# Performance work log

Measured on AMD Instinct MI355X. Metric: run time of the kernel, lower is better.

## Reference

```python
import jax, jax.numpy as jnp
import numpy as np

D_MODEL = 128
N_LAYERS = 2
D_STATE = 16
D_CONV = 4
EXPAND = 2
GRID = 16
D_INNER = D_MODEL * EXPAND
DT_RANK = (D_MODEL + 15) // 16  # mamba_ssm default: ceil(d_model/16) = 8
BATCH = 128
SEQ = 200


def setup_inputs() -> dict:
    key = jax.random.key(0)
    ks = jax.random.split(key, 24)
    L = N_LAYERS

    def rn(k, shape, scale=0.02):
        return jax.random.normal(k, shape, dtype=jnp.float32) * scale

    A_init = jnp.log(jnp.broadcast_to(
        jnp.arange(1, D_STATE + 1, dtype=jnp.float32), (L, D_INNER, D_STATE)))
    kan_scale = 1.0 / (np.sqrt(D_MODEL) * np.sqrt(GRID))
    return {
        "x": jax.random.normal(ks[0], (BATCH, SEQ, D_MODEL), dtype=jnp.float32),
        "in_w": rn(ks[1], (L, 2 * D_INNER, D_MODEL)),
        "out_w": rn(ks[2], (L, D_MODEL, D_INNER)),
        "conv_w_f": rn(ks[3], (L, D_INNER, D_CONV), 0.1),
        "conv_b_f": rn(ks[4], (L, D_INNER), 0.01),
        "conv_w_b": rn(ks[5], (L, D_INNER, D_CONV), 0.1),
        "conv_b_b": rn(ks[6], (L, D_INNER), 0.01),
        "xproj_w_f": rn(ks[7], (L, DT_RANK + 2 * D_STATE, D_INNER)),
        "xproj_w_b": rn(ks[8], (L, DT_RANK + 2 * D_STATE, D_INNER)),
        "dtproj_w_f": rn(ks[9], (L, D_INNER, DT_RANK), 0.1),
        "dtproj_b_f": rn(ks[10], (L, D_INNER), 0.01),
        "dtproj_w_b": rn(ks[11], (L, D_INNER, DT_RANK), 0.1),
        "dtproj_b_b": rn(ks[12], (L, D_INNER), 0.01),
        "A_log_f": A_init,
        "A_log_b": A_init,
        "D_f": jnp.ones((L, D_INNER), jnp.float32),
        "D_b": jnp.ones((L, D_INNER), jnp.float32),
        "ln1_w": jnp.ones((L, D_MODEL), jnp.float32),
        "ln1_b": jnp.zeros((L, D_MODEL), jnp.float32),
        "ln_w": jnp.ones((L, D_MODEL), jnp.float32),
        "ln_b": jnp.zeros((L, D_MODEL), jnp.float32),
        "kan_coef": jax.random.normal(ks[13], (L, 2, D_MODEL, D_MODEL, GRID), dtype=jnp.float32) * kan_scale,
    }


def _ln(x, w, b, eps=1e-12):
    u = x.mean(-1, keepdims=True)
    s = ((x - u) ** 2).mean(-1, keepdims=True)
    return w * (x - u) / jnp.sqrt(s + eps) + b


def _silu(x):
    return x * jax.nn.sigmoid(x)


def _mamba(x, in_w, out_w, conv_w, conv_b, xp_w, dt_w, dt_b, A_log, Dp):
    # x: (B, L, d_model). Faithful to mamba_ssm Mamba (bias=False proj, conv_bias=True).
    B, L, _ = x.shape
    xz = jnp.einsum('bld,ed->ble', x, in_w)          # (B, L, 2*d_inner)
    xi, z = jnp.split(xz, 2, axis=-1)
    # causal depthwise conv over L
    xp = jnp.pad(xi, ((0, 0), (D_CONV - 1, 0), (0, 0)))
    xc = sum(xp[:, k:k + L, :] * conv_w[:, k] for k in range(D_CONV)) + conv_b
    xc = _silu(xc)                                    # (B, L, d_inner)
    dbl = jnp.einsum('ble,fe->blf', xc, xp_w)         # (B, L, dt_rank+2*d_state)
    dt = jax.nn.softplus(
        jnp.einsum('blr,dr->bld', dbl[..., :DT_RANK], dt_w) + dt_b)
    Bm = dbl[..., DT_RANK:DT_RANK + D_STATE]          # (B, L, d_state)
    Cm = dbl[..., DT_RANK + D_STATE:]
    A = -jnp.exp(A_log)                               # (d_inner, d_state)

    def step(h, inp):
        dt_t, u_t, b_t, c_t = inp                     # (B,di),(B,di),(B,ds),(B,ds)
        h = jnp.exp(dt_t[:, :, None] * A) * h + (dt_t * u_t)[:, :, None] * b_t[:, None, :]
        return h, jnp.einsum('bds,bs->bd', h, c_t)

    h0 = jnp.zeros((B, D_INNER, D_STATE), x.dtype)
    _, ys = jax.lax.scan(step, h0, (jnp.moveaxis(dt, 1, 0), jnp.moveaxis(xc, 1, 0),
                                    jnp.moveaxis(Bm, 1, 0), jnp.moveaxis(Cm, 1, 0)))
    y = jnp.moveaxis(ys, 0, 1) + xc * Dp              # (B, L, d_inner)
    y = y * _silu(z)
    return jnp.einsum('ble,de->bld', y, out_w)


def _kan(x, coef):
    # coef: (2, outdim, inputdim, grid)
    shp = x.shape
    xf = x.reshape(-1, shp[-1])                       # (N, d)
    kk = jnp.arange(1, GRID + 1, dtype=x.dtype)
    ang = xf[:, :, None] * kk                         # (N, d, grid)
    y = (jnp.einsum('nig,jig->nj', jnp.cos(ang), coef[0])
         + jnp.einsum('nig,jig->nj', jnp.sin(ang), coef[1]))
    return y.reshape(shp[:-1] + (coef.shape[1],))


def reference(x, in_w, out_w, conv_w_f, conv_b_f, conv_w_b, conv_b_b,
              xproj_w_f, xproj_w_b, dtproj_w_f, dtproj_b_f, dtproj_w_b, dtproj_b_b,
              A_log_f, A_log_b, D_f, D_b, ln1_w, ln1_b, ln_w, ln_b, kan_coef):
    feats = []
    h = x
    for l in range(N_LAYERS):
        o = _ln(h, ln1_w[l], ln1_b[l])
        f = _mamba(o, in_w[l], out_w[l], conv_w_f[l], conv_b_f[l],
                   xproj_w_f[l], dtproj_w_f[l], dtproj_b_f[l], A_log_f[l], D_f[l])
        b = _mamba(o[:, ::-1], in_w[l], out_w[l], conv_w_b[l], conv_b_b[l],
                   xproj_w_b[l], dtproj_w_b[l], dtproj_b_b[l], A_log_b[l], D_b[l])[:, ::-1]
        o = _ln(f + b, ln_w[l], ln_b[l])
        o = _kan(o, kan_coef[l])  # dropout p=0.0 (eval) -> identity
        h = o + h
        feats.append(h)
    return sum(feats) / len(feats)
```

## Files before the change

### kernel.cpp

```cpp
#include <hip/hip_runtime.h>
#include <hip/hip_bf16.h>
#include <cmath>

#define BATCH 128
#define SEQ 200
#define DMODEL 128
#define DINNER 256
#define DSTATE 16
#define NTOK (BATCH * SEQ)

typedef __bf16 bf16x8 __attribute__((ext_vector_type(8)));
typedef float f32x4 __attribute__((ext_vector_type(4)));

__device__ __forceinline__ unsigned short f2bf(float f) {
  union { float f; unsigned u; } x{f};
  const unsigned r = x.u + 0x7fffu + ((x.u >> 16) & 1u);
  return (unsigned short)(r >> 16);
}
__device__ __forceinline__ float bf2f(unsigned short h) {
  union { unsigned u; float f; } x{(unsigned)h << 16};
  return x.f;
}
__device__ __forceinline__ void split2(float a, float b, unsigned& hp, unsigned& lp) {
  const unsigned short ha = f2bf(a), hb = f2bf(b);
  const float ra = a - bf2f(ha), rb = b - bf2f(hb);
  hp = (unsigned)ha | ((unsigned)hb << 16);
  lp = (unsigned)f2bf(ra) | ((unsigned)f2bf(rb) << 16);
}

template <int CTRL>
__device__ __forceinline__ float dpp_add(float v) {
  const int r = __builtin_amdgcn_update_dpp(0, __float_as_int(v), CTRL, 0xF, 0xF, true);
  return v + __int_as_float(r);
}

__device__ __forceinline__ float silu_f(float x) {
  return x / (1.f + __expf(-x));
}

__global__ __launch_bounds__(256) void ln_kernel(const float* __restrict__ in,
                                                 const float* __restrict__ w,
                                                 const float* __restrict__ b,
                                                 float* __restrict__ out) {
  const int wv = threadIdx.x >> 6;
  const int lane = threadIdx.x & 63;
  const int row = blockIdx.x * 4 + wv;
  const float2 v = *(const float2*)(in + (size_t)row * DMODEL + lane * 2);
  float s = v.x + v.y;
#pragma unroll
  for (int o = 32; o; o >>= 1) s += __shfl_xor(s, o, 64);
  const float u = s * (1.f / 128.f);
  const float dx = v.x - u, dy = v.y - u;
  float sq = dx * dx + dy * dy;
#pragma unroll
  for (int o = 32; o; o >>= 1) sq += __shfl_xor(sq, o, 64);
  const float inv = rsqrtf(sq * (1.f / 128.f) + 1e-12f);
  const float2 wv2 = *(const float2*)(w + lane * 2);
  const float2 bv2 = *(const float2*)(b + lane * 2);
  float2 o2v;
  o2v.x = fmaf(wv2.x, dx * inv, bv2.x);
  o2v.y = fmaf(wv2.y, dy * inv, bv2.y);
  *(float2*)(out + (size_t)row * DMODEL + lane * 2) = o2v;
}

__global__ __launch_bounds__(256) void wprep(const float* __restrict__ in_w,
                                             const float* __restrict__ xpwf,
                                             const float* __restrict__ xpwb,
                                             const float* __restrict__ out_w,
                                             unsigned short* __restrict__ iwH,
                                             unsigned short* __restrict__ iwL,
                                             unsigned short* __restrict__ xfH,
                                             unsigned short* __restrict__ xfL,
                                             unsigned short* __restrict__ xbH,
                                             unsigned short* __restrict__ xbL,
                                             unsigned short* __restrict__ owH,
                                             unsigned short* __restrict__ owL) {
  const int idx = blockIdx.x * 256 + threadIdx.x;
  float w;
  unsigned short *H, *L;
  int off;
  if (idx < 65536)      { w = in_w[idx];        H = iwH; L = iwL; off = idx; }
  else if (idx < 75776) { w = xpwf[idx - 65536]; H = xfH; L = xfL; off = idx - 65536; }
  else if (idx < 86016) { w = xpwb[idx - 75776]; H = xbH; L = xbL; off = idx - 75776; }
  else                  { w = out_w[idx - 86016]; H = owH; L = owL; off = idx - 86016; }
  const unsigned short h = f2bf(w);
  H[off] = h;
  L[off] = f2bf(w - bf2f(h));
}

template <int MODE>
__global__ __launch_bounds__(256) void gemm_c(const float* __restrict__ A1,
                                              const float* __restrict__ A2,
                                              const float* __restrict__ Zp,
                                              const unsigned short* __restrict__ Whi,
                                              const unsigned short* __restrict__ Wlo,
                                              float* __restrict__ C,
                                              const unsigned short* __restrict__ Whi2,
                                              const unsigned short* __restrict__ Wlo2,
                                              float* __restrict__ C2,
                                              int M, int N, int K) {
  __shared__ unsigned short AshH[64 * 40], AshL[64 * 40];
  __shared__ unsigned short BshH[128 * 40], BshL[128 * 40];
  const float* Ause = A1;
  const unsigned short* WH = Whi;
  const unsigned short* WL = Wlo;
  float* Cuse = C;
  if (MODE == 2 && blockIdx.z == 1) { Ause = A2; WH = Whi2; WL = Wlo2; Cuse = C2; }
  const int tid = threadIdx.x;
  const int m0 = blockIdx.y * 64;
  const int n0 = blockIdx.x * 128;
  const int lane = tid & 63;
  const int wid = tid >> 6;
  const int arow = lane & 15;
  const int kch = (lane >> 4) * 8;
  const int bcol = wid * 32 + (lane & 15);
  f32x4 acc[4][2] = {};
  for (int k0 = 0; k0 < K; k0 += 32) {
    __syncthreads();
    {
      const int row = tid >> 2;
      const int koff = (tid & 3) * 8;
      const int m = m0 + row;
      float4 v0 = *(const float4*)(Ause + (size_t)m * K + k0 + koff);
      float4 v1 = *(const float4*)(Ause + (size_t)m * K + k0 + koff + 4);
      if (MODE == 1) {
        const float4 u0 = *(const float4*)(A2 + (size_t)m * K + k0 + koff);
        const float4 u1 = *(const float4*)(A2 + (size_t)m * K + k0 + koff + 4);
        const float4 z0 = *(const float4*)(Zp + (size_t)m * 512 + k0 + koff);
        const float4 z1 = *(const float4*)(Zp + (size_t)m * 512 + k0 + koff + 4);
        v0.x = (v0.x + u0.x) * silu_f(z0.x);
        v0.y = (v0.y + u0.y) * silu_f(z0.y);
        v0.z = (v0.z + u0.z) * silu_f(z0.z);
        v0.w = (v0.w + u0.w) * silu_f(z0.w);
        v1.x = (v1.x + u1.x) * silu_f(z1.x);
        v1.y = (v1.y + u1.y) * silu_f(z1.y);
        v1.z = (v1.z + u1.z) * silu_f(z1.z);
        v1.w = (v1.w + u1.w) * silu_f(z1.w);
      }
      unsigned h0, l0, h1, l1, h2, l2, h3, l3;
      split2(v0.x, v0.y, h0, l0);
      split2(v0.z, v0.w, h1, l1);
      split2(v1.x, v1.y, h2, l2);
      split2(v1.z, v1.w, h3, l3);
      *(uint4*)&AshH[row * 40 + koff] = make_uint4(h0, h1, h2, h3);
      *(uint4*)&AshL[row * 40 + koff] = make_uint4(l0, l1, l2, l3);
    }
    {
      const int row = tid >> 1;
      const int koff = (tid & 1) * 16;
      const int n = n0 + row;
      uint4 wh0 = make_uint4(0, 0, 0, 0), wh1 = wh0, wl0 = wh0, wl1 = wh0;
      if (n < N) {
        wh0 = *(const uint4*)(WH + (size_t)n * K + k0 + koff);
        wh1 = *(const uint4*)(WH + (size_t)n * K + k0 + koff + 8);
        wl0 = *(const uint4*)(WL + (size_t)n * K + k0 + koff);
        wl1 = *(const uint4*)(WL + (size_t)n * K + k0 + koff + 8);
      }
      *(uint4*)&BshH[row * 40 + koff] = wh0;
      *(uint4*)&BshH[row * 40 + koff + 8] = wh1;
      *(uint4*)&BshL[row * 40 + koff] = wl0;
      *(uint4*)&BshL[row * 40 + koff + 8] = wl1;
    }
    __syncthreads();
    const bf16x8 bh0 = *(const bf16x8*)&BshH[bcol * 40 + kch];
    const bf16x8 bh1 = *(const bf16x8*)&BshH[(bcol + 16) * 40 + kch];
    const bf16x8 bl0 = *(const bf16x8*)&BshL[bcol * 40 + kch];
    const bf16x8 bl1 = *(const bf16x8*)&BshL[(bcol + 16) * 40 + kch];
#pragma unroll
    for (int g = 0; g < 4; ++g) {
      const bf16x8 ah = *(const bf16x8*)&AshH[(g * 16 + arow) * 40 + kch];
      const bf16x8 al = *(const bf16x8*)&AshL[(g * 16 + arow) * 40 + kch];
      acc[g][0] = __builtin_amdgcn_mfma_f32_16x16x32_bf16(ah, bh0, acc[g][0], 0, 0, 0);
      acc[g][0] = __builtin_amdgcn_mfma_f32_16x16x32_bf16(al, bh0, acc[g][0], 0, 0, 0);
      acc[g][0] = __builtin_amdgcn_mfma_f32_16x16x32_bf16(ah, bl0, acc[g][0], 0, 0, 0);
      acc[g][1] = __builtin_amdgcn_mfma_f32_16x16x32_bf16(ah, bh1, acc[g][1], 0, 0, 0);
      acc[g][1] = __builtin_amdgcn_mfma_f32_16x16x32_bf16(al, bh1, acc[g][1], 0, 0, 0);
      acc[g][1] = __builtin_amdgcn_mfma_f32_16x16x32_bf16(ah, bl1, acc[g][1], 0, 0, 0);
    }
  }
  const int q0 = (lane >> 4) * 4;
#pragma unroll
  for (int g = 0; g < 4; ++g)
#pragma unroll
    for (int fc = 0; fc < 2; ++fc)
#pragma unroll
      for (int q = 0; q < 4; ++q) {
        const int m = m0 + g * 16 + q0 + q;
        const int n = n0 + wid * 32 + fc * 16 + (lane & 15);
        if (n < N) Cuse[(size_t)m * N + n] = acc[g][fc][q];
      }
}

__global__ __launch_bounds__(256) void conv_silu_kernel(const float* __restrict__ xz,
                                                        const float* __restrict__ cwf,
                                                        const float* __restrict__ cbf,
                                                        const float* __restrict__ cwb,
                                                        const float* __restrict__ cbb,
                                                        float* __restrict__ xcf,
                                                        float* __restrict__ xcb) {
  const int n0 = blockIdx.x * 8;
  const int l0 = n0 % SEQ;
  const int e = threadIdx.x;
  const float4 wf = *(const float4*)(cwf + e * 4);
  const float4 wb = *(const float4*)(cwb + e * 4);
  const float bfv = cbf[e], bbv = cbb[e];
  const float* px = xz + (size_t)n0 * 512 + e;
  float w[7];
#pragma unroll
  for (int j = 0; j < 6; ++j) {
    const int l = l0 - 3 + j;
    w[j] = (l >= 0 && l < SEQ) ? px[(j - 3) * 512] : 0.f;
  }
#pragma unroll
  for (int t = 0; t < 8; ++t) {
    const int l = l0 + t;
    w[6] = (l + 3 < SEQ) ? px[(t + 3) * 512] : 0.f;
    const float af = fmaf(wf.x, w[0], fmaf(wf.y, w[1], fmaf(wf.z, w[2], fmaf(wf.w, w[3], bfv))));
    const float ab = fmaf(wb.x, w[6], fmaf(wb.y, w[5], fmaf(wb.z, w[4], fmaf(wb.w, w[3], bbv))));
    xcf[(size_t)(n0 + t) * DINNER + e] = silu_f(af);
    xcb[(size_t)(n0 + t) * DINNER + e] = silu_f(ab);
#pragma unroll
    for (int j = 0; j < 6; ++j) w[j] = w[j + 1];
  }
}

__global__ __launch_bounds__(256) void dtsp_kernel2(const float* __restrict__ dblF,
                                                    const float* __restrict__ dblB,
                                                    const float* __restrict__ dtwF,
                                                    const float* __restrict__ dtbF,
                                                    const float* __restrict__ dtwB,
                                                    const float* __restrict__ dtbB,
                                                    float* __restrict__ dtF,
                                                    float* __restrict__ dtB) {
  const int bwd = blockIdx.y;
  const float* __restrict__ dbl = bwd ? dblB : dblF;
  const float* __restrict__ dtw = bwd ? dtwB : dtwF;
  const float* __restrict__ dtb = bwd ? dtbB : dtbF;
  float* __restrict__ dt = bwd ? dtB : dtF;
  __shared__ float r[8][8];
  const int n0 = blockIdx.x * 8;
  const int d = threadIdx.x;
  if (threadIdx.x < 64) {
    const int tt = threadIdx.x >> 3, j = threadIdx.x & 7;
    r[tt][j] = dbl[(size_t)(n0 + tt) * 40 + j];
  }
  const float4 w0 = *(const float4*)(dtw + d * 8);
  const float4 w1 = *(const float4*)(dtw + d * 8 + 4);
  const float bd = dtb[d];
  __syncthreads();
#pragma unroll
  for (int tt = 0; tt < 8; ++tt) {
    float acc = bd;
    acc += r[tt][0] * w0.x + r[tt][1] * w0.y + r[tt][2] * w0.z + r[tt][3] * w0.w;
    acc += r[tt][4] * w1.x + r[tt][5] * w1.y + r[tt][6] * w1.z + r[tt][7] * w1.w;
    const float sp = acc > 20.f ? acc : log1pf(__expf(acc));
    dt[(size_t)(n0 + tt) * DINNER + d] = sp;
  }
}

__global__ __launch_bounds__(256) void scan_kernel3(
    const float* __restrict__ dtF, float* xcF, const float* __restrict__ dblF,
    const float* __restrict__ AlogF, const float* __restrict__ DF,
    const float* __restrict__ dtB, float* xcB, const float* __restrict__ dblB,
    const float* __restrict__ AlogB, const float* __restrict__ DB) {
  const int bwd = blockIdx.z;
  const float* __restrict__ dt = bwd ? dtB : dtF;
  float* xc = bwd ? xcB : xcF;
  const float* __restrict__ dbl = bwd ? dblB : dblF;
  const float* __restrict__ Alog = bwd ? AlogB : AlogF;
  const float* __restrict__ Dp = bwd ? DB : DF;
  const int bb = blockIdx.y;
  const int lane = threadIdx.x & 63;
  const int wid = threadIdx.x >> 6;
  const int q = lane & 3;
  const int dl = lane >> 2;
  const int d = blockIdx.x * 64 + wid * 16 + dl;
  const float LOG2E = 1.44269504f;
  const float4 al = *(const float4*)(Alog + d * DSTATE + q * 4);
  const float4 A2 = make_float4(-__expf(al.x) * LOG2E, -__expf(al.y) * LOG2E,
                                -__expf(al.z) * LOG2E, -__expf(al.w) * LOG2E);
  const float Dd = Dp[d];
  const int t0 = bwd ? (SEQ - 1) : 0;
  const ptrdiff_t sX = bwd ? -DINNER : DINNER;
  const ptrdiff_t sB = bwd ? -40 : 40;
  const float* pdt = dt + (size_t)(bb * SEQ + t0) * DINNER + d;
  float* pxc = xc + (size_t)(bb * SEQ + t0) * DINNER + d;
  const float* pbc = dbl + (size_t)(bb * SEQ + t0) * 40 + 8 + q * 4;
  float4 h = make_float4(0.f, 0.f, 0.f, 0.f);
#pragma unroll 2
  for (int t = 0; t < SEQ; ++t) {
    const float dtv = *pdt;
    const float u = *pxc;
    const float4 Bv = *(const float4*)pbc;
    const float4 Cv = *(const float4*)(pbc + 16);
    const float du = dtv * u;
    float4 a;
    a.x = exp2f(dtv * A2.x);
    a.y = exp2f(dtv * A2.y);
    a.z = exp2f(dtv * A2.z);
    a.w = exp2f(dtv * A2.w);
    h.x = fmaf(a.x, h.x, du * Bv.x);
    h.y = fmaf(a.y, h.y, du * Bv.y);
    h.z = fmaf(a.z, h.z, du * Bv.z);
    h.w = fmaf(a.w, h.w, du * Bv.w);
    float pp = fmaf(h.w, Cv.w, fmaf(h.z, Cv.z, fmaf(h.y, Cv.y, h.x * Cv.x)));
    pp = dpp_add<0xB1>(pp);
    pp = dpp_add<0x4E>(pp);
    if (q == 0) *pxc = fmaf(u, Dd, pp);
    pdt += sX;
    pxc += sX;
    pbc += sB;
  }
}

__global__ __launch_bounds__(256) void kan_prep(const float* __restrict__ coef,
                                                unsigned short* __restrict__ Wt) {
  const int idx = blockIdx.x * 256 + threadIdx.x;
  const int k = idx & 31;
  const int j = (idx >> 5) & 127;
  const int i = idx >> 12;
  const int c = k >> 4, g = k & 15;
  Wt[idx] = f2bf(coef[(((size_t)c * 128 + j) * 128 + i) * 16 + g]);
}

__global__ __launch_bounds__(256) void kan_mfma(const float* __restrict__ x,
                                                const unsigned short* __restrict__ Wt,
                                                const float* __restrict__ hin,
                                                float* __restrict__ hout,
                                                float* __restrict__ accum,
                                                int first) {
  __shared__ float Xs[128 * 64];
  __shared__ unsigned short F[2][64 * 40];
  __shared__ unsigned short Wsh[2][128 * 40];
  const int tid = threadIdx.x;
  const int n0 = blockIdx.x * 64;
  const int wid = tid >> 6;
  const int lane = tid & 63;
  {
    const int tok = tid & 63;
    const int cq = tid >> 6;
#pragma unroll
    for (int r = 0; r < 8; ++r) {
      const int i0 = cq * 32 + r * 4;
      const float4 v = *(const float4*)(x + (size_t)(n0 + tok) * 128 + i0);
      Xs[(i0 + 0) * 64 + tok] = v.x;
      Xs[(i0 + 1) * 64 + tok] = v.y;
      Xs[(i0 + 2) * 64 + tok] = v.z;
      Xs[(i0 + 3) * 64 + tok] = v.w;
    }
  }
  const int fs = tid >> 7;
  const int fn = (tid & 127) >> 1;
  const int fh = tid & 1;
  const int wrow = tid & 127;
  const int arow = lane & 15;
  const int kch = (lane >> 4) * 8;
  const int bcol = wid * 32 + (lane & 15);
  f32x4 acc[4][2] = {};
  for (int ii = 0; ii < 128; ii += 2) {
    __syncthreads();
    {
      const uint4* src = (const uint4*)(Wt + (size_t)(ii + fs) * 4096 + wrow * 32);
      uint4* dst = (uint4*)&Wsh[fs][wrow * 40];
      dst[0] = src[0]; dst[1] = src[1]; dst[2] = src[2]; dst[3] = src[3];
    }
    {
      const float xv = Xs[(ii + fs) * 64 + fn];
      const float c1 = __cosf(xv), s1 = __sinf(xv);
      float c, s;
      if (fh == 0) { c = c1; s = s1; }
      else {
        const float y = xv * 9.f;
        c = __cosf(y); s = __sinf(y);
      }
      unsigned int* Fu = (unsigned int*)F[fs];
#pragma unroll
      for (int p = 0; p < 4; ++p) {
        const float c2 = c * c1 - s * s1;
        const float s2 = s * c1 + c * s1;
        Fu[fn * 20 + fh * 4 + p]     = (unsigned)f2bf(c) | ((unsigned)f2bf(c2) << 16);
        Fu[fn * 20 + 8 + fh * 4 + p] = (unsigned)f2bf(s) | ((unsigned)f2bf(s2) << 16);
        c = c2 * c1 - s2 * s1;
        s = s2 * c1 + c2 * s1;
      }
    }
    __syncthreads();
#pragma unroll
    for (int sl = 0; sl < 2; ++sl) {
      const bf16x8 b0 = *(const bf16x8*)&Wsh[sl][bcol * 40 + kch];
      const bf16x8 b1 = *(const bf16x8*)&Wsh[sl][(bcol + 16) * 40 + kch];
#pragma unroll
      for (int g = 0; g < 4; ++g) {
        const bf16x8 a = *(const bf16x8*)&F[sl][(g * 16 + arow) * 40 + kch];
        acc[g][0] = __builtin_amdgcn_mfma_f32_16x16x32_bf16(a, b0, acc[g][0], 0, 0, 0);
        acc[g][1] = __builtin_amdgcn_mfma_f32_16x16x32_bf16(a, b1, acc[g][1], 0, 0, 0);
      }
    }
  }
  const int q0 = (lane >> 4) * 4;
#pragma unroll
  for (int g = 0; g < 4; ++g)
#pragma unroll
    for (int fc = 0; fc < 2; ++fc)
#pragma unroll
      for (int q = 0; q < 4; ++q) {
        const int n = n0 + g * 16 + q0 + q;
        const int j = wid * 32 + fc * 16 + (lane & 15);
        const size_t off = (size_t)n * 128 + j;
        const float v = acc[g][fc][q] + hin[off];
        hout[off] = v;
        const float a = 0.5f * v;
        accum[off] = first ? a : (accum[off] + a);
      }
}

extern "C" void kernel_launch(void* const* d_in, const int* in_sizes, int n_in,
                              void* d_out, int out_size, void* d_ws, size_t ws_size,
                              hipStream_t stream) {
  (void)in_sizes; (void)n_in; (void)out_size;
  const float* x     = (const float*)d_in[0];
  const float* in_w  = (const float*)d_in[1];
  const float* out_w = (const float*)d_in[2];
  const float* cwf   = (const float*)d_in[3];
  const float* cbf   = (const float*)d_in[4];
  const float* cwb   = (const float*)d_in[5];
  const float* cbb   = (const float*)d_in[6];
  const float* xpwf  = (const float*)d_in[7];
  const float* xpwb  = (const float*)d_in[8];
  const float* dtwf  = (const float*)d_in[9];
  const float* dtbf  = (const float*)d_in[10];
  const float* dtwb  = (const float*)d_in[11];
  const float* dtbb  = (const float*)d_in[12];
  const float* Alogf = (const float*)d_in[13];
  const float* Alogb = (const float*)d_in[14];
  const float* Dfp   = (const float*)d_in[15];
  const float* Dbp   = (const float*)d_in[16];
  const float* ln1w  = (const float*)d_in[17];
  const float* ln1b  = (const float*)d_in[18];
  const float* lnw   = (const float*)d_in[19];
  const float* lnb   = (const float*)d_in[20];
  const float* kanc  = (const float*)d_in[21];
  float* outp = (float*)d_out;

  int C = 128;
  while (C > 8) {
    const size_t need = ((size_t)643072 + (size_t)2000 * C * SEQ) * 4;
    if (need <= ws_size) break;
    C >>= 1;
  }
  const int T = C * SEQ;

  float* p = (float*)d_ws;
  unsigned short* Wt2  = (unsigned short*)p; p += 524288;
  unsigned short* pl   = (unsigned short*)p; p += 118784;
  float* o1   = p; p += (size_t)T * 128;
  float* xzb  = p; p += (size_t)T * 512;
  float* xcf  = p; p += (size_t)T * 256;
  float* xcb  = p; p += (size_t)T * 256;
  float* dblf = p; p += (size_t)T * 40;
  float* dblb = p; p += (size_t)T * 40;
  float* dtf  = p; p += (size_t)T * 256;
  float* dtb  = p; p += (size_t)T * 256;
  float* o2   = p; p += (size_t)T * 128;
  float* hbuf = p; p += (size_t)T * 128;

  unsigned short* Wt_l[2];
  unsigned short *iwH[2], *iwL[2], *xfH[2], *xfL[2], *xbH[2], *xbL[2], *owH[2], *owL[2];
  for (int l = 0; l < 2; ++l) {
    Wt_l[l] = Wt2 + (size_t)l * 524288;
    unsigned short* q = pl + (size_t)l * 118784;
    iwH[l] = q;          iwL[l] = q + 32768;
    xfH[l] = q + 65536;  xfL[l] = q + 70656;
    xbH[l] = q + 75776;  xbL[l] = q + 80896;
    owH[l] = q + 86016;  owL[l] = q + 102400;
  }
  for (int l = 0; l < 2; ++l) {
    unsigned short* q = pl + (size_t)l * 118784 * 2;
    (void)q;
  }
  {
    unsigned short* base = (unsigned short*)d_ws;
    unsigned short* plbase = base + 2 * 524288;
    for (int l = 0; l < 2; ++l) {
      unsigned short* q = plbase + (size_t)l * 237568;
      iwH[l] = q;           iwL[l] = q + 65536;
      xfH[l] = q + 131072;  xfL[l] = q + 141312;
      xbH[l] = q + 151552;  xbL[l] = q + 161792;
      owH[l] = q + 172032;  owL[l] = q + 204800;
    }
  }
  {
    float* pf = (float*)d_ws + 761856;
    o1   = pf; pf += (size_t)T * 128;
    xzb  = pf; pf += (size_t)T * 512;
    xcf  = pf; pf += (size_t)T * 256;
    xcb  = pf; pf += (size_t)T * 256;
    dblf = pf; pf += (size_t)T * 40;
    dblb = pf; pf += (size_t)T * 40;
    dtf  = pf; pf += (size_t)T * 256;
    dtb  = pf; pf += (size_t)T * 256;
    o2   = pf; pf += (size_t)T * 128;
    hbuf = pf; pf += (size_t)T * 128;
  }

  for (int l = 0; l < 2; ++l) {
    wprep<<<464, 256, 0, stream>>>(in_w + (size_t)l * 65536, xpwf + (size_t)l * 10240,
                                   xpwb + (size_t)l * 10240, out_w + (size_t)l * 32768,
                                   iwH[l], iwL[l], xfH[l], xfL[l],
                                   xbH[l], xbL[l], owH[l], owL[l]);
    kan_prep<<<2048, 256, 0, stream>>>(kanc + (size_t)l * 2 * 128 * 128 * 16, Wt_l[l]);
  }

  for (int b0 = 0; b0 < BATCH; b0 += C) {
    const size_t tok0 = (size_t)b0 * SEQ;
    for (int l = 0; l < 2; ++l) {
      const float* hin = (l == 0) ? (x + tok0 * 128) : hbuf;
      ln_kernel<<<T / 4, 256, 0, stream>>>(hin, ln1w + l * 128, ln1b + l * 128, o1);
      gemm_c<0><<<dim3(4, T / 64), 256, 0, stream>>>(
          o1, (const float*)nullptr, (const float*)nullptr,
          iwH[l], iwL[l], xzb,
          (const unsigned short*)nullptr, (const unsigned short*)nullptr,
          (float*)nullptr, T, 512, 128);
      conv_silu_kernel<<<T / 8, 256, 0, stream>>>(xzb, cwf + l * 1024, cbf + l * 256,
                                                  cwb + l * 1024, cbb + l * 256, xcf, xcb);
      gemm_c<2><<<dim3(1, T / 64, 2), 256, 0, stream>>>(
          xcf, xcb, (const float*)nullptr,
          xfH[l], xfL[l], dblf, xbH[l], xbL[l], dblb, T, 40, 256);
      dtsp_kernel2<<<dim3(T / 8, 2), 256, 0, stream>>>(dblf, dblb,
                                                       dtwf + l * 2048, dtbf + l * 256,
                                                       dtwb + l * 2048, dtbb + l * 256,
                                                       dtf, dtb);
      scan_kernel3<<<dim3(4, C, 2), 256, 0, stream>>>(
          dtf, xcf, dblf, Alogf + l * 4096, Dfp + l * 256,
          dtb, xcb, dblb, Alogb + l * 4096, Dbp + l * 256);
      gemm_c<1><<<dim3(1, T / 64), 256, 0, stream>>>(
          xcf, xcb, xzb + 256, owH[l], owL[l], o1,
          (const unsigned short*)nullptr, (const unsigned short*)nullptr,
          (float*)nullptr, T, 128, 256);
      ln_kernel<<<T / 4, 256, 0, stream>>>(o1, lnw + l * 128, lnb + l * 128, o2);
      kan_mfma<<<T / 64, 256, 0, stream>>>(o2, Wt_l[l], hin, hbuf,
                                           outp + tok0 * 128, l == 0 ? 1 : 0);
    }
  }
}
```

Before: 650.0 us.

## Fuse out-projection GEMM with LayerNorm and template scan direction

The out-projection GEMM (with the gating multiply) now also applies the following LayerNorm through a shared-memory tile, so o1 is no longer written to and re-read from global memory and one launch per layer goes away. The scan kernel is rewritten as a templated body with compile-time strides, split per direction and unrolled by 4, so addresses are computed as constants and loads can be issued ahead. The host-side workspace setup is also cleaned up. The fused kernel uses about 34 KB more LDS for its output tile, which may reduce occupancy.

```diff
diff --git a/kernel.cpp b/kernel.cpp
--- a/kernel.cpp
+++ b/kernel.cpp
@@ -91,7 +91,6 @@
 template <int MODE>
 __global__ __launch_bounds__(256) void gemm_c(const float* __restrict__ A1,
                                               const float* __restrict__ A2,
-                                              const float* __restrict__ Zp,
                                               const unsigned short* __restrict__ Whi,
                                               const unsigned short* __restrict__ Wlo,
                                               float* __restrict__ C,
@@ -123,20 +122,6 @@
       const int m = m0 + row;
       float4 v0 = *(const float4*)(Ause + (size_t)m * K + k0 + koff);
       float4 v1 = *(const float4*)(Ause + (size_t)m * K + k0 + koff + 4);
-      if (MODE == 1) {
-        const float4 u0 = *(const float4*)(A2 + (size_t)m * K + k0 + koff);
-        const float4 u1 = *(const float4*)(A2 + (size_t)m * K + k0 + koff + 4);
-        const float4 z0 = *(const float4*)(Zp + (size_t)m * 512 + k0 + koff);
-        const float4 z1 = *(const float4*)(Zp + (size_t)m * 512 + k0 + koff + 4);
-        v0.x = (v0.x + u0.x) * silu_f(z0.x);
-        v0.y = (v0.y + u0.y) * silu_f(z0.y);
-        v0.z = (v0.z + u0.z) * silu_f(z0.z);
-        v0.w = (v0.w + u0.w) * silu_f(z0.w);
-        v1.x = (v1.x + u1.x) * silu_f(z1.x);
-        v1.y = (v1.y + u1.y) * silu_f(z1.y);
-        v1.z = (v1.z + u1.z) * silu_f(z1.z);
-        v1.w = (v1.w + u1.w) * silu_f(z1.w);
-      }
       unsigned h0, l0, h1, l1, h2, l2, h3, l3;
       split2(v0.x, v0.y, h0, l0);
       split2(v0.z, v0.w, h1, l1);
@@ -189,6 +174,127 @@
         const int n = n0 + wid * 32 + fc * 16 + (lane & 15);
         if (n < N) Cuse[(size_t)m * N + n] = acc[g][fc][q];
       }
+}
+
+__global__ __launch_bounds__(256) void gemm_oln(const float* __restrict__ A1,
+                                                const float* __restrict__ A2v,
+                                                const float* __restrict__ Zp,
+                                                const unsigned short* __restrict__ Whi,
+                                                const unsigned short* __restrict__ Wlo,
+                                                const float* __restrict__ lw,
+                                                const float* __restrict__ lb,
+                                                float* __restrict__ o2out) {
+  __shared__ unsigned short AshH[64 * 40], AshL[64 * 40];
+  __shared__ unsigned short BshH[128 * 40], BshL[128 * 40];
+  __shared__ float Csh[64][132];
+  const int tid = threadIdx.x;
+  const int m0 = blockIdx.x * 64;
+  const int lane = tid & 63;
+  const int wid = tid >> 6;
+  const int arow = lane & 15;
+  const int kch = (lane >> 4) * 8;
+  const int bcol = wid * 32 + (lane & 15);
+  f32x4 acc[4][2] = {};
+  for (int k0 = 0; k0 < 256; k0 += 32) {
+    __syncthreads();
+    {
+      const int row = tid >> 2;
+      const int koff = (tid & 3) * 8;
+      const int m = m0 + row;
+      float4 v0 = *(const float4*)(A1 + (size_t)m * 256 + k0 + koff);
+      float4 v1 = *(const float4*)(A1 + (size_t)m * 256 + k0 + koff + 4);
+      const float4 u0 = *(const float4*)(A2v + (size_t)m * 256 + k0 + koff);
+      const float4 u1 = *(const float4*)(A2v + (size_t)m * 256 + k0 + koff + 4);
+      const float4 z0 = *(const float4*)(Zp + (size_t)m * 512 + k0 + koff);
+      const float4 z1 = *(const float4*)(Zp + (size_t)m * 512 + k0 + koff + 4);
+      v0.x = (v0.x + u0.x) * silu_f(z0.x);
+      v0.y = (v0.y + u0.y) * silu_f(z0.y);
+      v0.z = (v0.z + u0.z) * silu_f(z0.z);
+      v0.w = (v0.w + u0.w) * silu_f(z0.w);
+      v1.x = (v1.x + u1.x) * silu_f(z1.x);
+      v1.y = (v1.y + u1.y) * silu_f(z1.y);
+      v1.z = (v1.z + u1.z) * silu_f(z1.z);
+      v1.w = (v1.w + u1.w) * silu_f(z1.w);
+      unsigned h0, l0, h1, l1, h2, l2, h3, l3;
+      split2(v0.x, v0.y, h0, l0);
+      split2(v0.z, v0.w, h1, l1);
+      split2(v1.x, v1.y, h2, l2);
+      split2(v1.z, v1.w, h3, l3);
+      *(uint4*)&AshH[row * 40 + koff] = make_uint4(h0, h1, h2, h3);
+      *(uint4*)&AshL[row * 40 + koff] = make_uint4(l0, l1, l2, l3);
+    }
+    {
+      const int row = tid >> 1;
+      const int koff = (tid & 1) * 16;
+      const uint4 wh0 = *(const uint4*)(Whi + (size_t)row * 256 + k0 + koff);
+      const uint4 wh1 = *(const uint4*)(Whi + (size_t)row * 256 + k0 + koff + 8);
+      const uint4 wl0 = *(const uint4*)(Wlo + (size_t)row * 256 + k0 + koff);
+      const uint4 wl1 = *(const uint4*)(Wlo + (size_t)row * 256 + k0 + koff + 8);
+      *(uint4*)&BshH[row * 40 + koff] = wh0;
+      *(uint4*)&BshH[row * 40 + koff + 8] = wh1;
+      *(uint4*)&BshL[row * 40 + koff] = wl0;
+      *(uint4*)&BshL[row * 40 + koff + 8] = wl1;
+    }
+    __syncthreads();
+    const bf16x8 bh0 = *(const bf16x8*)&BshH[bcol * 40 + kch];
+    const bf16x8 bh1 = *(const bf16x8*)&BshH[(bcol + 16) * 40 + kch];
+    const bf16x8 bl0 = *(const bf16x8*)&BshL[bcol * 40 + kch];
+    const bf16x8 bl1 = *(const bf16x8*)&BshL[(bcol + 16) * 40 + kch];
+#pragma unroll
+    for (int g = 0; g < 4; ++g) {
+      const bf16x8 ah = *(const bf16x8*)&AshH[(g * 16 + arow) * 40 + kch];
+      const bf16x8 al = *(const bf16x8*)&AshL[(g * 16 + arow) * 40 + kch];
+      acc[g][0] = __builtin_amdgcn_mfma_f32_16x16x32_bf16(ah, bh0, acc[g][0], 0, 0, 0);
+      acc[g][0] = __builtin_amdgcn_mfma_f32_16x16x32_bf16(al, bh0, acc[g][0], 0, 0, 0);
+      acc[g][0] = __builtin_amdgcn_mfma_f32_16x16x32_bf16(ah, bl0, acc[g][0], 0, 0, 0);
+      acc[g][1] = __builtin_amdgcn_mfma_f32_16x16x32_bf16(ah, bh1, acc[g][1], 0, 0, 0);
+      acc[g][1] = __builtin_amdgcn_mfma_f32_16x16x32_bf16(al, bh1, acc[g][1], 0, 0, 0);
+      acc[g][1] = __builtin_amdgcn_mfma_f32_16x16x32_bf16(ah, bl1, acc[g][1], 0, 0, 0);
+    }
+  }
+  __syncthreads();
+  const int q0 = (lane >> 4) * 4;
+#pragma unroll
+  for (int g = 0; g < 4; ++g)
+#pragma unroll
+    for (int fc = 0; fc < 2; ++fc)
+#pragma unroll
+      for (int q = 0; q < 4; ++q)
+        Csh[g * 16 + q0 + q][wid * 32 + fc * 16 + (lane & 15)] = acc[g][fc][q];
+  __syncthreads();
+  const int row = tid >> 2;
+  const int c0 = (tid & 3) * 32;
+  float vloc[32];
+  float s = 0.f;
+#pragma unroll
+  for (int j = 0; j < 32; ++j) {
+    vloc[j] = Csh[row][c0 + j];
+    s += vloc[j];
+  }
+  s = dpp_add<0xB1>(s);
+  s = dpp_add<0x4E>(s);
+  const float u = s * (1.f / 128.f);
+  float sq = 0.f;
+#pragma unroll
+  for (int j = 0; j < 32; ++j) {
+    const float dd = vloc[j] - u;
+    sq += dd * dd;
+  }
+  sq = dpp_add<0xB1>(sq);
+  sq = dpp_add<0x4E>(sq);
+  const float inv = rsqrtf(sq * (1.f / 128.f) + 1e-12f);
+  float* outp = o2out + (size_t)(m0 + row) * 128 + c0;
+#pragma unroll
+  for (int j4 = 0; j4 < 8; ++j4) {
+    const float4 wv = *(const float4*)(lw + c0 + j4 * 4);
+    const float4 bv = *(const float4*)(lb + c0 + j4 * 4);
+    float4 o;
+    o.x = fmaf(wv.x, (vloc[j4 * 4 + 0] - u) * inv, bv.x);
+    o.y = fmaf(wv.y, (vloc[j4 * 4 + 1] - u) * inv, bv.y);
+    o.z = fmaf(wv.z, (vloc[j4 * 4 + 2] - u) * inv, bv.z);
+    o.w = fmaf(wv.w, (vloc[j4 * 4 + 3] - u) * inv, bv.w);
+    *(float4*)(outp + j4 * 4) = o;
+  }
 }
 
 __global__ __launch_bounds__(256) void conv_silu_kernel(const float* __restrict__ xz,
@@ -258,18 +364,13 @@
   }
 }
 
-__global__ __launch_bounds__(256) void scan_kernel3(
-    const float* __restrict__ dtF, float* xcF, const float* __restrict__ dblF,
-    const float* __restrict__ AlogF, const float* __restrict__ DF,
-    const float* __restrict__ dtB, float* xcB, const float* __restrict__ dblB,
-    const float* __restrict__ AlogB, const float* __restrict__ DB) {
-  const int bwd = blockIdx.z;
-  const float* __restrict__ dt = bwd ? dtB : dtF;
-  float* xc = bwd ? xcB : xcF;
-  const float* __restrict__ dbl = bwd ? dblB : dblF;
-  const float* __restrict__ Alog = bwd ? AlogB : AlogF;
-  const float* __restrict__ Dp = bwd ? DB : DF;
-  const int bb = blockIdx.y;
+template <int SX, int SB>
+__device__ __forceinline__ void scan_body(const float* __restrict__ dt,
+                                          float* __restrict__ xc,
+                                          const float* __restrict__ dbl,
+                                          const float* __restrict__ Alog,
+                                          const float* __restrict__ Dp,
+                                          int bb) {
   const int lane = threadIdx.x & 63;
   const int wid = threadIdx.x >> 6;
   const int q = lane & 3;
@@ -280,37 +381,46 @@
   const float4 A2 = make_float4(-__expf(al.x) * LOG2E, -__expf(al.y) * LOG2E,
                                 -__expf(al.z) * LOG2E, -__expf(al.w) * LOG2E);
   const float Dd = Dp[d];
-  const int t0 = bwd ? (SEQ - 1) : 0;
-  const ptrdiff_t sX = bwd ? -DINNER : DINNER;
-  const ptrdiff_t sB = bwd ? -40 : 40;
-  const float* pdt = dt + (size_t)(bb * SEQ + t0) * DINNER + d;
-  float* pxc = xc + (size_t)(bb * SEQ + t0) * DINNER + d;
-  const float* pbc = dbl + (size_t)(bb * SEQ + t0) * 40 + 8 + q * 4;
+  const int t0 = (SX > 0) ? 0 : (SEQ - 1);
+  int offX = (bb * SEQ + t0) * DINNER + d;
+  int offB = (bb * SEQ + t0) * 40 + 8 + q * 4;
   float4 h = make_float4(0.f, 0.f, 0.f, 0.f);
-#pragma unroll 2
-  for (int t = 0; t < SEQ; ++t) {
-    const float dtv = *pdt;
-    const float u = *pxc;
-    const float4 Bv = *(const float4*)pbc;
-    const float4 Cv = *(const float4*)(pbc + 16);
-    const float du = dtv * u;
-    float4 a;
-    a.x = exp2f(dtv * A2.x);
-    a.y = exp2f(dtv * A2.y);
-    a.z = exp2f(dtv * A2.z);
-    a.w = exp2f(dtv * A2.w);
-    h.x = fmaf(a.x, h.x, du * Bv.x);
-    h.y = fmaf(a.y, h.y, du * Bv.y);
-    h.z = fmaf(a.z, h.z, du * Bv.z);
-    h.w = fmaf(a.w, h.w, du * Bv.w);
-    float pp = fmaf(h.w, Cv.w, fmaf(h.z, Cv.z, fmaf(h.y, Cv.y, h.x * Cv.x)));
-    pp = dpp_add<0xB1>(pp);
-    pp = dpp_add<0x4E>(pp);
-    if (q == 0) *pxc = fmaf(u, Dd, pp);
-    pdt += sX;
-    pxc += sX;
-    pbc += sB;
-  }
+  for (int t = 0; t < SEQ; t += 4) {
+#pragma unroll
+    for (int k = 0; k < 4; ++k) {
+      const float dtv = dt[offX + k * SX];
+      const float u = xc[offX + k * SX];
+      const float4 Bv = *(const float4*)(dbl + offB + k * SB);
+      const float4 Cv = *(const float4*)(dbl + offB + k * SB + 16);
+      const float du = dtv * u;
+      float4 a;
+      a.x = exp2f(dtv * A2.x);
+      a.y = exp2f(dtv * A2.y);
+      a.z = exp2f(dtv * A2.z);
+      a.w = exp2f(dtv * A2.w);
+      h.x = fmaf(a.x, h.x, du * Bv.x);
+      h.y = fmaf(a.y, h.y, du * Bv.y);
+      h.z = fmaf(a.z, h.z, du * Bv.z);
+      h.w = fmaf(a.w, h.w, du * Bv.w);
+      float pp = fmaf(h.w, Cv.w, fmaf(h.z, Cv.z, fmaf(h.y, Cv.y, h.x * Cv.x)));
+      pp = dpp_add<0xB1>(pp);
+      pp = dpp_add<0x4E>(pp);
+      if (q == 0) xc[offX + k * SX] = fmaf(u, Dd, pp);
+    }
+    offX += 4 * SX;
+    offB += 4 * SB;
+  }
+}
+
+__global__ __launch_bounds__(256) void scan_kernel4(
+    const float* __restrict__ dtF, float* xcF, const float* __restrict__ dblF,
+    const float* __restrict__ AlogF, const float* __restrict__ DF,
+    const float* __restrict__ dtB, float* xcB, const float* __restrict__ dblB,
+    const float* __restrict__ AlogB, const float* __restrict__ DB) {
+  if (blockIdx.z == 0)
+    scan_body<DINNER, 40>(dtF, xcF, dblF, AlogF, DF, blockIdx.y);
+  else
+    scan_body<-DINNER, -40>(dtB, xcB, dblB, AlogB, DB, blockIdx.y);
 }
 
 __global__ __launch_bounds__(256) void kan_prep(const float* __restrict__ coef,
@@ -444,64 +554,34 @@
 
   int C = 128;
   while (C > 8) {
-    const size_t need = ((size_t)643072 + (size_t)2000 * C * SEQ) * 4;
+    const size_t need = ((size_t)761856 + (size_t)2000 * C * SEQ) * 4;
     if (need <= ws_size) break;
     C >>= 1;
   }
   const int T = C * SEQ;
 
-  float* p = (float*)d_ws;
-  unsigned short* Wt2  = (unsigned short*)p; p += 524288;
-  unsigned short* pl   = (unsigned short*)p; p += 118784;
-  float* o1   = p; p += (size_t)T * 128;
-  float* xzb  = p; p += (size_t)T * 512;
-  float* xcf  = p; p += (size_t)T * 256;
-  float* xcb  = p; p += (size_t)T * 256;
-  float* dblf = p; p += (size_t)T * 40;
-  float* dblb = p; p += (size_t)T * 40;
-  float* dtf  = p; p += (size_t)T * 256;
-  float* dtb  = p; p += (size_t)T * 256;
-  float* o2   = p; p += (size_t)T * 128;
-  float* hbuf = p; p += (size_t)T * 128;
-
+  unsigned short* usbase = (unsigned short*)d_ws;
   unsigned short* Wt_l[2];
   unsigned short *iwH[2], *iwL[2], *xfH[2], *xfL[2], *xbH[2], *xbL[2], *owH[2], *owL[2];
   for (int l = 0; l < 2; ++l) {
-    Wt_l[l] = Wt2 + (size_t)l * 524288;
-    unsigned short* q = pl + (size_t)l * 118784;
-    iwH[l] = q;          iwL[l] = q + 32768;
-    xfH[l] = q + 65536;  xfL[l] = q + 70656;
-    xbH[l] = q + 75776;  xbL[l] = q + 80896;
-    owH[l] = q + 86016;  owL[l] = q + 102400;
-  }
-  for (int l = 0; l < 2; ++l) {
-    unsigned short* q = pl + (size_t)l * 118784 * 2;
-    (void)q;
-  }
-  {
-    unsigned short* base = (unsigned short*)d_ws;
-    unsigned short* plbase = base + 2 * 524288;
-    for (int l = 0; l < 2; ++l) {
-      unsigned short* q = plbase + (size_t)l * 237568;
-      iwH[l] = q;           iwL[l] = q + 65536;
-      xfH[l] = q + 131072;  xfL[l] = q + 141312;
-      xbH[l] = q + 151552;  xbL[l] = q + 161792;
-      owH[l] = q + 172032;  owL[l] = q + 204800;
-    }
-  }
-  {
-    float* pf = (float*)d_ws + 761856;
-    o1   = pf; pf += (size_t)T * 128;
-    xzb  = pf; pf += (size_t)T * 512;
-    xcf  = pf; pf += (size_t)T * 256;
-    xcb  = pf; pf += (size_t)T * 256;
-    dblf = pf; pf += (size_t)T * 40;
-    dblb = pf; pf += (size_t)T * 40;
-    dtf  = pf; pf += (size_t)T * 256;
-    dtb  = pf; pf += (size_t)T * 256;
-    o2   = pf; pf += (size_t)T * 128;
-    hbuf = pf; pf += (size_t)T * 128;
-  }
+    Wt_l[l] = usbase + (size_t)l * 524288;
+    unsigned short* q = usbase + 2 * 524288 + (size_t)l * 237568;
+    iwH[l] = q;           iwL[l] = q + 65536;
+    xfH[l] = q + 131072;  xfL[l] = q + 141312;
+    xbH[l] = q + 151552;  xbL[l] = q + 161792;
+    owH[l] = q + 172032;  owL[l] = q + 204800;
+  }
+  float* pf = (float*)d_ws + 761856;
+  float* o1   = pf; pf += (size_t)T * 128;
+  float* xzb  = pf; pf += (size_t)T * 512;
+  float* xcf  = pf; pf += (size_t)T * 256;
+  float* xcb  = pf; pf += (size_t)T * 256;
+  float* dblf = pf; pf += (size_t)T * 40;
+  float* dblb = pf; pf += (size_t)T * 40;
+  float* dtf  = pf; pf += (size_t)T * 256;
+  float* dtb  = pf; pf += (size_t)T * 256;
+  float* o2   = pf; pf += (size_t)T * 128;
+  float* hbuf = pf; pf += (size_t)T * 128;
 
   for (int l = 0; l < 2; ++l) {
     wprep<<<464, 256, 0, stream>>>(in_w + (size_t)l * 65536, xpwf + (size_t)l * 10240,
@@ -517,27 +597,22 @@
       const float* hin = (l == 0) ? (x + tok0 * 128) : hbuf;
       ln_kernel<<<T / 4, 256, 0, stream>>>(hin, ln1w + l * 128, ln1b + l * 128, o1);
       gemm_c<0><<<dim3(4, T / 64), 256, 0, stream>>>(
-          o1, (const float*)nullptr, (const float*)nullptr,
-          iwH[l], iwL[l], xzb,
+          o1, (const float*)nullptr, iwH[l], iwL[l], xzb,
           (const unsigned short*)nullptr, (const unsigned short*)nullptr,
           (float*)nullptr, T, 512, 128);
       conv_silu_kernel<<<T / 8, 256, 0, stream>>>(xzb, cwf + l * 1024, cbf + l * 256,
                                                   cwb + l * 1024, cbb + l * 256, xcf, xcb);
       gemm_c<2><<<dim3(1, T / 64, 2), 256, 0, stream>>>(
-          xcf, xcb, (const float*)nullptr,
-          xfH[l], xfL[l], dblf, xbH[l], xbL[l], dblb, T, 40, 256);
+          xcf, xcb, xfH[l], xfL[l], dblf, xbH[l], xbL[l], dblb, T, 40, 256);
       dtsp_kernel2<<<dim3(T / 8, 2), 256, 0, stream>>>(dblf, dblb,
                                                        dtwf + l * 2048, dtbf + l * 256,
                                                        dtwb + l * 2048, dtbb + l * 256,
                                                        dtf, dtb);
-      scan_kernel3<<<dim3(4, C, 2), 256, 0, stream>>>(
+      scan_kernel4<<<dim3(4, C, 2), 256, 0, stream>>>(
           dtf, xcf, dblf, Alogf + l * 4096, Dfp + l * 256,
           dtb, xcb, dblb, Alogb + l * 4096, Dbp + l * 256);
-      gemm_c<1><<<dim3(1, T / 64), 256, 0, stream>>>(
-          xcf, xcb, xzb + 256, owH[l], owL[l], o1,
-          (const unsigned short*)nullptr, (const unsigned short*)nullptr,
-          (float*)nullptr, T, 128, 256);
-      ln_kernel<<<T / 4, 256, 0, stream>>>(o1, lnw + l * 128, lnb + l * 128, o2);
+      gemm_oln<<<T / 64, 256, 0, stream>>>(xcf, xcb, xzb + 256, owH[l], owL[l],
+                                           lnw + l * 128, lnb + l * 128, o2);
       kan_mfma<<<T / 64, 256, 0, stream>>>(o2, Wt_l[l], hin, hbuf,
                                            outp + tok0 * 128, l == 0 ? 1 : 0);
     }
```

New measurement: 636.8 us. -2.0%, faster.
